# Kernel optimization log

Hardware: AMD Instinct MI355X
Metric: run time of the kernel (lower is better)

The kernel has to match this reference:

```python
import jax, jax.numpy as jnp
import numpy as np

HEADS = 8
DIM_HEAD = 40
SCALE = DIM_HEAD ** -0.5


def setup_inputs() -> dict:
    key = jax.random.key(0)
    ks = jax.random.split(key, 6)
    B, S, D = 2, 4096, 320  # batch, seq (64x64 latent), query_dim
    inner = HEADS * DIM_HEAD  # 320
    s = 0.02
    return {
        "x": jax.random.normal(ks[0], (B, S, D), jnp.float32),
        "Wq": jax.random.normal(ks[1], (inner, D), jnp.float32) * s,
        "Wk": jax.random.normal(ks[2], (inner, D), jnp.float32) * s,
        "Wv": jax.random.normal(ks[3], (inner, D), jnp.float32) * s,
        "Wout": jax.random.normal(ks[4], (D, inner), jnp.float32) * s,
        "bout": jnp.zeros((D,), jnp.float32),
    }


def _split_heads(t):
    # [B, S, h*d] -> [B, h, S, d]
    B, S, _ = t.shape
    return t.reshape(B, S, HEADS, DIM_HEAD).transpose(0, 2, 1, 3)


def reference(x, Wq, Wk, Wv, Wout, bout):
    # self-attention path (context=None): k/v come from x
    q = _split_heads(x @ Wq.T)  # [B,h,S,d]
    k = _split_heads(x @ Wk.T)
    v = _split_heads(x @ Wv.T)
    # scores: materialized O(S^2) attention as in the torch einsum
    attn = jax.nn.softmax(jnp.einsum('bhid,bhjd->bhij', q, k) * SCALE, axis=-1)
    out = jnp.einsum('bhij,bhjd->bhid', attn, v)  # [B,h,S,d]
    B, _, S, _ = out.shape
    out = out.transpose(0, 2, 1, 3).reshape(B, S, HEADS * DIM_HEAD)
    return out @ Wout.T + bout  # to_out (dropout=0 -> identity)
```

## Files before the change

kernel.cpp:

```cpp
#include <hip/hip_runtime.h>

#define HEADS 8
#define DHEAD 40
#define SEQ   4096
#define BATCH 2
#define INNER 320
#define NBH   16
#define QSCALE ((float)(0.15811388300841897 * 1.4426950408889634))

typedef _Float16 f16;
typedef __attribute__((ext_vector_type(2)))  __fp16   fp16x2;
typedef __attribute__((ext_vector_type(4)))  _Float16 half4;
typedef __attribute__((ext_vector_type(8)))  _Float16 half8;
typedef __attribute__((ext_vector_type(16))) float    f32x16;

#if __has_builtin(__builtin_amdgcn_exp2f)
#define EXP2F(x) __builtin_amdgcn_exp2f(x)
#else
#define EXP2F(x) exp2f(x)
#endif

#define MFMA16(a, b, c) __builtin_amdgcn_mfma_f32_32x32x16_f16(a, b, c, 0, 0, 0)

union H8 { half8 h8; fp16x2 p2[4]; uint4 u4; };

#define WQKV4 (3 * INNER * INNER / 4)
#define WOUT4 (INNER * INNER / 4)
#define WTOT4 (WQKV4 + WOUT4)

__global__ __launch_bounds__(256)
void convert_kernel(const float* __restrict__ Wq,
                    const float* __restrict__ Wk,
                    const float* __restrict__ Wv,
                    const float* __restrict__ Wout,
                    f16* __restrict__ wh, f16* __restrict__ wouth)
{
    int i = blockIdx.x * 256 + threadIdx.x;
    if (i >= WTOT4) return;
    float4 v;
    f16* dst;
    float sc = 1.0f;
    if (i < WQKV4) {
        if (i < 25600)      { v = ((const float4*)Wq)[i]; sc = QSCALE; }
        else if (i < 51200) { v = ((const float4*)Wk)[i - 25600]; }
        else                { v = ((const float4*)Wv)[i - 51200]; }
        dst = wh + 4 * (size_t)i;
    } else {
        int j = i - WQKV4;
        v = ((const float4*)Wout)[j];
        dst = wouth + 4 * (size_t)j;
    }
    H8 u;
    u.p2[0] = __builtin_amdgcn_cvt_pkrtz(v.x * sc, v.y * sc);
    u.p2[1] = __builtin_amdgcn_cvt_pkrtz(v.z * sc, v.w * sc);
    *(uint2*)dst = make_uint2(u.u4.x, u.u4.y);
}

#define QSTR 72

__global__ __launch_bounds__(256)
void qkv_gemm_kernel(const float* __restrict__ x, const f16* __restrict__ wh,
                     f16* __restrict__ q, f16* __restrict__ k,
                     f16* __restrict__ vt)
{
    __shared__ f16 lds[(64 + 192) * QSTR];
    f16* As = lds;
    f16* Bs = lds + 64 * QSTR;

    const int tid = threadIdx.x;
    const int nb0 = blockIdx.x * 64;
    const int m0  = blockIdx.y * 64;
    const int wave = tid >> 6, lane = tid & 63, m = lane & 31, half = lane >> 5;
    const int mw = wave >> 1, nw = wave & 1;

    f32x16 acc[3];
    #pragma unroll
    for (int i = 0; i < 16; i++) { acc[0][i] = 0.f; acc[1][i] = 0.f; acc[2][i] = 0.f; }

    for (int k0 = 0; k0 < 320; k0 += 64) {
        __syncthreads();
        #pragma unroll
        for (int u = 0; u < 2; u++) {
            int idx = tid + 256 * u;
            int r = idx >> 3, c8 = idx & 7;
            const float* xr = &x[(size_t)(m0 + r) * 320 + k0 + c8 * 8];
            float4 v0 = *(const float4*)xr;
            float4 v1 = *(const float4*)(xr + 4);
            H8 hh;
            hh.p2[0] = __builtin_amdgcn_cvt_pkrtz(v0.x, v0.y);
            hh.p2[1] = __builtin_amdgcn_cvt_pkrtz(v0.z, v0.w);
            hh.p2[2] = __builtin_amdgcn_cvt_pkrtz(v1.x, v1.y);
            hh.p2[3] = __builtin_amdgcn_cvt_pkrtz(v1.z, v1.w);
            *(uint4*)&As[r * QSTR + c8 * 8] = hh.u4;
        }
        #pragma unroll
        for (int u = 0; u < 6; u++) {
            int idx = tid + 256 * u;
            int r = idx >> 3, c8 = idx & 7;
            int wr = (r >> 6) * 320 + nb0 + (r & 63);
            *(uint4*)&Bs[r * QSTR + c8 * 8] =
                *(const uint4*)&wh[(size_t)wr * 320 + k0 + c8 * 8];
        }
        __syncthreads();
        #pragma unroll
        for (int c = 0; c < 4; c++) {
            half8 a = *(const half8*)&As[(mw * 32 + m) * QSTR + c * 16 + half * 8];
            #pragma unroll
            for (int t = 0; t < 3; t++) {
                half8 bf = *(const half8*)&Bs[(nw * 96 + t * 32 + m) * QSTR + c * 16 + half * 8];
                acc[t] = MFMA16(a, bf, acc[t]);
            }
        }
    }

    const int b = m0 >> 12, s0 = m0 & 4095;

    #pragma unroll
    for (int t = 0; t < 3; t++) {
        int st = nw * 3 + t;
        if (st < 4) {
            f16* dst = (st < 2) ? q : k;
            int col = nb0 + (st & 1) * 32 + m;
            int h  = (col * 205) >> 13;
            int dd = col - h * 40;
            #pragma unroll
            for (int reg = 0; reg < 16; reg++) {
                int crow = 4 * half + (reg & 3) + 8 * (reg >> 2);
                int mg = m0 + mw * 32 + crow;
                int bb = mg >> 12, s = mg & 4095;
                dst[((size_t)(bb * 8 + h) * SEQ + s) * DHEAD + dd] = (f16)acc[t][reg];
            }
        }
    }

    __syncthreads();
    f16* Ct = lds;
    if (nw == 1) {
        #pragma unroll
        for (int t = 1; t < 3; t++) {
            int vr0 = (t - 1) * 32 + m;
            #pragma unroll
            for (int g = 0; g < 4; g++) {
                half4 hh;
                hh.x = (f16)acc[t][4 * g + 0]; hh.y = (f16)acc[t][4 * g + 1];
                hh.z = (f16)acc[t][4 * g + 2]; hh.w = (f16)acc[t][4 * g + 3];
                *(half4*)&Ct[vr0 * QSTR + mw * 32 + 8 * g + 4 * half] = hh;
            }
        }
    }
    __syncthreads();
    #pragma unroll
    for (int u = 0; u < 4; u++) {
        int idx = tid + 256 * u;
        int rl = idx >> 4, c4 = idx & 15;
        int col = nb0 + rl;
        int h  = (col * 205) >> 13;
        int dd = col - h * 40;
        int w4 = c4 & 3;
        int c4p = (c4 & ~3) | ((w4 == 1) ? 2 : (w4 == 2) ? 1 : w4);
        *(uint2*)&vt[((size_t)(b * 8 + h) * DHEAD + dd) * SEQ + s0 + c4p * 4] =
            *(const uint2*)&Ct[rl * QSTR + c4 * 4];
    }
}

__global__ __launch_bounds__(512, 4)
void attn_kernel(const f16* __restrict__ q, const f16* __restrict__ k,
                 const f16* __restrict__ vt, f16* __restrict__ y)
{
    __shared__ __align__(16) unsigned char ldsbuf[33792];
    f16*   ldsh = (f16*)ldsbuf;
    float* ldsf = (float*)ldsbuf;

    const int tid = threadIdx.x;
    const int blk = blockIdx.x;
    const int xcd = blk & 7, slot = blk >> 3;
    const int bh = xcd * 2 + (slot >> 5), qt = slot & 31;
    const int b = bh >> 3, h = bh & 7;
    const int q0 = qt * 128;
    const int wave = tid >> 6, lane = tid & 63, m = lane & 31, half = lane >> 5;
    const int qp = wave >> 1, kh = wave & 1;
    const int x7 = m & 7;

    if (tid < 128) {
        int bsel = tid >> 6, r = tid & 63;
        *(uint4*)&ldsh[bsel * 8192 + r * 64 + 8 * (5 ^ (r & 7))] = make_uint4(0, 0, 0, 0);
    } else {
        int idx = tid - 128;
        int bsel = (idx >= 192) ? 1 : 0;
        int j = idx - bsel * 192;
        int r = 40 + (j >> 3), c = j & 7;
        uint4 val = (r == 40) ? make_uint4(0x3C003C00u, 0x3C003C00u, 0x3C003C00u, 0x3C003C00u)
                              : make_uint4(0, 0, 0, 0);
        *(uint4*)&ldsh[bsel * 8192 + 4096 + r * 64 + 8 * (c ^ (r & 7))] = val;
    }

    half8 zero8;
    #pragma unroll
    for (int j = 0; j < 8; j++) zero8[j] = (f16)0.0f;

    half8 qa[3];
    {
        const f16* qb = q + ((size_t)bh * SEQ + q0 + qp * 32 + m) * DHEAD;
        qa[0] = *(const half8*)&qb[half * 8];
        qa[1] = *(const half8*)&qb[16 + half * 8];
        qa[2] = (half == 1) ? zero8 : *(const half8*)&qb[32];
    }

    f32x16 O0, O1;
    #pragma unroll
    for (int i = 0; i < 16; i++) { O0[i] = 0.f; O1[i] = 0.f; }

    const f16* kb = k  + (size_t)bh * SEQ * DHEAD;
    const f16* vb = vt + (size_t)bh * DHEAD * SEQ;

    const bool aIsK = (tid < 320);
    int adst, astep;
    const f16* aptr;
    if (aIsK) {
        int r = (tid * 205) >> 10, c = tid - r * 5;
        adst = r * 64 + 8 * (c ^ (r & 7));
        aptr = kb + (size_t)r * DHEAD + c * 8;
        astep = 64 * DHEAD;
    } else {
        int t = tid - 320;
        int r = t >> 3, c = t & 7;
        adst = 4096 + r * 64 + 8 * (c ^ (r & 7));
        aptr = vb + (size_t)r * SEQ + c * 8;
        astep = 64;
    }
    const bool hasB = (tid < 128);
    int bdst = 0;
    const f16* bptr = vb;
    if (hasB) {
        int t = 192 + tid;
        int r = t >> 3, c = t & 7;
        bdst = 4096 + r * 64 + 8 * (c ^ (r & 7));
        bptr = vb + (size_t)r * SEQ + c * 8;
    }

    uint4 sA = *(const uint4*)aptr;
    uint4 sB = make_uint4(0, 0, 0, 0);
    if (hasB) sB = *(const uint4*)bptr;

    for (int j0 = 0; j0 < SEQ; j0 += 64) {
        const int stg = ((j0 >> 6) & 1) * 8192;
        *(uint4*)&ldsh[stg + adst] = sA;
        if (hasB) *(uint4*)&ldsh[stg + bdst] = sB;
        __syncthreads();

        if (j0 + 64 < SEQ) {
            aptr += astep;
            sA = *(const uint4*)aptr;
            if (hasB) { bptr += 64; sB = *(const uint4*)bptr; }
        }

        const f16* Kb = &ldsh[stg];
        const f16* Vb = &ldsh[stg + 4096];

        half8 kf[3];
        #pragma unroll
        for (int c = 0; c < 3; c++)
            kf[c] = *(const half8*)&Kb[(kh * 32 + m) * 64 + 8 * ((2 * c + half) ^ x7)];

        f32x16 S;
        #pragma unroll
        for (int i = 0; i < 16; i++) S[i] = 0.f;
        __builtin_amdgcn_s_setprio(1);
        S = MFMA16(kf[0], qa[0], S);
        S = MFMA16(kf[1], qa[1], S);
        S = MFMA16(kf[2], qa[2], S);
        __builtin_amdgcn_s_setprio(0);

        half8 vf[2][2];
        #pragma unroll
        for (int c = 0; c < 2; c++) {
            vf[c][0] = *(const half8*)&Vb[m * 64        + 8 * ((4 * kh + 2 * c + half) ^ x7)];
            vf[c][1] = *(const half8*)&Vb[(32 + m) * 64 + 8 * ((4 * kh + 2 * c + half) ^ x7)];
        }

        H8 p0, p1;
        #pragma unroll
        for (int g = 0; g < 4; g++) {
            p0.p2[g] = __builtin_amdgcn_cvt_pkrtz(EXP2F(S[2 * g]),     EXP2F(S[2 * g + 1]));
            p1.p2[g] = __builtin_amdgcn_cvt_pkrtz(EXP2F(S[8 + 2 * g]), EXP2F(S[9 + 2 * g]));
        }

        __builtin_amdgcn_s_setprio(1);
        O0 = MFMA16(p0.h8, vf[0][0], O0);
        O1 = MFMA16(p0.h8, vf[0][1], O1);
        O0 = MFMA16(p1.h8, vf[1][0], O0);
        O1 = MFMA16(p1.h8, vf[1][1], O1);
        __builtin_amdgcn_s_setprio(0);
    }

    __syncthreads();
    if (kh == 1) {
        #pragma unroll
        for (int reg = 0; reg < 16; reg++) {
            int row = 4 * half + (reg & 3) + 8 * (reg >> 2);
            ldsf[(qp * 32 + row) * 66 + m]      = O0[reg];
            ldsf[(qp * 32 + row) * 66 + 32 + m] = O1[reg];
        }
    }
    __syncthreads();
    if (kh == 0) {
        #pragma unroll
        for (int reg = 0; reg < 16; reg++) {
            int row = 4 * half + (reg & 3) + 8 * (reg >> 2);
            O0[reg] += ldsf[(qp * 32 + row) * 66 + m];
            O1[reg] += ldsf[(qp * 32 + row) * 66 + 32 + m];
        }
        #pragma unroll
        for (int reg = 0; reg < 16; reg++) {
            float l = __shfl(O1[reg], 8 + 32 * half, 64);
            float rinv = 1.0f / l;
            int row = 4 * half + (reg & 3) + 8 * (reg >> 2);
            f16* yr = y + ((size_t)b * SEQ + q0 + qp * 32 + row) * INNER + h * DHEAD;
            yr[m] = (f16)(O0[reg] * rinv);
            if (m < 8) yr[32 + m] = (f16)(O1[reg] * rinv);
        }
    }
}

#define ASTR 72

__global__ __launch_bounds__(256)
void out_proj_kernel(const f16* __restrict__ y, const f16* __restrict__ wouth,
                     const float* __restrict__ bout, float* __restrict__ out)
{
    __shared__ f16 lds[(128 + 64) * ASTR];
    f16* As = lds;
    f16* Bs = lds + 128 * ASTR;

    const int tid = threadIdx.x;
    const int m0 = blockIdx.y * 128;
    const int n0 = blockIdx.x * 64;
    const int wave = tid >> 6, lane = tid & 63, m = lane & 31, half = lane >> 5;

    f32x16 acc[2];
    #pragma unroll
    for (int i = 0; i < 16; i++) { acc[0][i] = 0.f; acc[1][i] = 0.f; }

    for (int k0 = 0; k0 < 320; k0 += 64) {
        __syncthreads();
        #pragma unroll
        for (int u = 0; u < 4; u++) {
            int idx = tid + 256 * u;
            int r = idx >> 3, c8 = idx & 7;
            *(uint4*)&As[r * ASTR + c8 * 8] =
                *(const uint4*)&y[(size_t)(m0 + r) * 320 + k0 + c8 * 8];
        }
        #pragma unroll
        for (int u = 0; u < 2; u++) {
            int idx = tid + 256 * u;
            int r = idx >> 3, c8 = idx & 7;
            *(uint4*)&Bs[r * ASTR + c8 * 8] =
                *(const uint4*)&wouth[(size_t)(n0 + r) * 320 + k0 + c8 * 8];
        }
        __syncthreads();
        #pragma unroll
        for (int c = 0; c < 4; c++) {
            half8 a  = *(const half8*)&As[(wave * 32 + m) * ASTR + c * 16 + half * 8];
            half8 b0 = *(const half8*)&Bs[m * ASTR + c * 16 + half * 8];
            half8 b1 = *(const half8*)&Bs[(32 + m) * ASTR + c * 16 + half * 8];
            acc[0] = MFMA16(a, b0, acc[0]);
            acc[1] = MFMA16(a, b1, acc[1]);
        }
    }

    #pragma unroll
    for (int nt = 0; nt < 2; nt++) {
        int n = n0 + nt * 32 + m;
        float bias = bout[n];
        #pragma unroll
        for (int reg = 0; reg < 16; reg++) {
            int crow = 4 * half + (reg & 3) + 8 * (reg >> 2);
            out[(size_t)(m0 + wave * 32 + crow) * 320 + n] = acc[nt][reg] + bias;
        }
    }
}

extern "C" void kernel_launch(void* const* d_in, const int* in_sizes, int n_in,
                              void* d_out, int out_size, void* d_ws, size_t ws_size,
                              hipStream_t stream)
{
    const float* x    = (const float*)d_in[0];
    const float* Wq   = (const float*)d_in[1];
    const float* Wk   = (const float*)d_in[2];
    const float* Wv   = (const float*)d_in[3];
    const float* Wout = (const float*)d_in[4];
    const float* bout = (const float*)d_in[5];
    float* out = (float*)d_out;

    unsigned char* ws = (unsigned char*)d_ws;
    f16* wh    = (f16*)(ws);
    f16* wouth = (f16*)(ws +   614400);
    f16* qd    = (f16*)(ws +   819200);
    f16* kd    = (f16*)(ws +  6062080);
    f16* vtd   = (f16*)(ws + 11304960);
    f16* yd    = (f16*)(ws + 16547840);

    convert_kernel <<<400,          256, 0, stream>>>(Wq, Wk, Wv, Wout, wh, wouth);
    qkv_gemm_kernel<<<dim3(5, 128), 256, 0, stream>>>(x, wh, qd, kd, vtd);
    attn_kernel    <<<512,          512, 0, stream>>>(qd, kd, vtd, yd);
    out_proj_kernel<<<dim3(5, 64),  256, 0, stream>>>(yd, wouth, bout, out);
}
```

Before: 159.5 us.

## Double KV tile to 128 keys per iteration in attention loop

Each attention-loop iteration now stages 128 keys instead of 64, so each wave computes two 32-key score blocks and runs eight PV MFMAs per barrier. The aim is to halve the number of __syncthreads and loop iterations and give more independent MFMA work to overlap with exp. In exchange, LDS grows from 33 KB to 64 KB per block and register pressure rises, which may cut occupancy below the declared 4 blocks per CU.

```diff
diff --git a/kernel.cpp b/kernel.cpp
--- a/kernel.cpp
+++ b/kernel.cpp
@@ -167,7 +167,7 @@
 void attn_kernel(const f16* __restrict__ q, const f16* __restrict__ k,
                  const f16* __restrict__ vt, f16* __restrict__ y)
 {
-    __shared__ __align__(16) unsigned char ldsbuf[33792];
+    __shared__ __align__(16) unsigned char ldsbuf[65536];
     f16*   ldsh = (f16*)ldsbuf;
     float* ldsf = (float*)ldsbuf;
 
@@ -181,17 +181,25 @@
     const int qp = wave >> 1, kh = wave & 1;
     const int x7 = m & 7;
 
-    if (tid < 128) {
-        int bsel = tid >> 6, r = tid & 63;
-        *(uint4*)&ldsh[bsel * 8192 + r * 64 + 8 * (5 ^ (r & 7))] = make_uint4(0, 0, 0, 0);
-    } else {
-        int idx = tid - 128;
-        int bsel = (idx >= 192) ? 1 : 0;
-        int j = idx - bsel * 192;
-        int r = 40 + (j >> 3), c = j & 7;
-        uint4 val = (r == 40) ? make_uint4(0x3C003C00u, 0x3C003C00u, 0x3C003C00u, 0x3C003C00u)
-                              : make_uint4(0, 0, 0, 0);
-        *(uint4*)&ldsh[bsel * 8192 + 4096 + r * 64 + 8 * (c ^ (r & 7))] = val;
+    if (tid < 256) {
+        int bsel = tid >> 7, r = tid & 127;
+        *(uint4*)&ldsh[bsel * 16384 + r * 64 + 8 * (5 ^ (r & 7))] = make_uint4(0, 0, 0, 0);
+    }
+    {
+        int idx = tid;
+        #pragma unroll
+        for (int pass = 0; pass < 2; pass++) {
+            if (pass == 0 || tid < 256) {
+                int bsel = (idx >= 384) ? 1 : 0;
+                int j = idx - 384 * bsel;
+                int r = 40 + (j >> 4), c = j & 15;
+                uint4 val = (r == 40) ? make_uint4(0x3C003C00u, 0x3C003C00u, 0x3C003C00u, 0x3C003C00u)
+                                      : make_uint4(0, 0, 0, 0);
+                *(uint4*)&ldsh[bsel * 16384 + 8192 + r * 128
+                               + 8 * ((c & 8) | ((c & 7) ^ (r & 7)))] = val;
+            }
+            idx = 512 + tid;
+        }
     }
 
     half8 zero8;
@@ -213,83 +221,100 @@
     const f16* kb = k  + (size_t)bh * SEQ * DHEAD;
     const f16* vb = vt + (size_t)bh * DHEAD * SEQ;
 
-    const bool aIsK = (tid < 320);
-    int adst, astep;
-    const f16* aptr;
-    if (aIsK) {
-        int r = (tid * 205) >> 10, c = tid - r * 5;
-        adst = r * 64 + 8 * (c ^ (r & 7));
-        aptr = kb + (size_t)r * DHEAD + c * 8;
-        astep = 64 * DHEAD;
+    int r0s = (tid * 205) >> 10, c0s = tid - r0s * 5;
+    const int d0 = r0s * 64 + 8 * (c0s ^ (r0s & 7));
+    const f16* p0 = kb + (size_t)r0s * DHEAD + c0s * 8;
+
+    int d1; const f16* p1; int st1;
+    if (tid < 128) {
+        int s = 512 + tid;
+        int r = (s * 205) >> 10, c = s - r * 5;
+        d1 = r * 64 + 8 * (c ^ (r & 7));
+        p1 = kb + (size_t)r * DHEAD + c * 8;
+        st1 = 128 * DHEAD;
     } else {
-        int t = tid - 320;
-        int r = t >> 3, c = t & 7;
-        adst = 4096 + r * 64 + 8 * (c ^ (r & 7));
-        aptr = vb + (size_t)r * SEQ + c * 8;
-        astep = 64;
-    }
-    const bool hasB = (tid < 128);
-    int bdst = 0;
-    const f16* bptr = vb;
-    if (hasB) {
-        int t = 192 + tid;
-        int r = t >> 3, c = t & 7;
-        bdst = 4096 + r * 64 + 8 * (c ^ (r & 7));
-        bptr = vb + (size_t)r * SEQ + c * 8;
-    }
-
-    uint4 sA = *(const uint4*)aptr;
-    uint4 sB = make_uint4(0, 0, 0, 0);
-    if (hasB) sB = *(const uint4*)bptr;
-
-    for (int j0 = 0; j0 < SEQ; j0 += 64) {
-        const int stg = ((j0 >> 6) & 1) * 8192;
-        *(uint4*)&ldsh[stg + adst] = sA;
-        if (hasB) *(uint4*)&ldsh[stg + bdst] = sB;
+        int t = tid - 128;
+        int r = t >> 4, c = t & 15;
+        d1 = 8192 + r * 128 + 8 * ((c & 8) | ((c & 7) ^ (r & 7)));
+        p1 = vb + (size_t)r * SEQ + c * 8;
+        st1 = 128;
+    }
+    const bool has2 = (tid < 256);
+    int d2 = 0; const f16* p2 = vb;
+    if (has2) {
+        int t = 384 + tid;
+        int r = t >> 4, c = t & 15;
+        d2 = 8192 + r * 128 + 8 * ((c & 8) | ((c & 7) ^ (r & 7)));
+        p2 = vb + (size_t)r * SEQ + c * 8;
+    }
+
+    uint4 s0v = *(const uint4*)p0;
+    uint4 s1v = *(const uint4*)p1;
+    uint4 s2v = make_uint4(0, 0, 0, 0);
+    if (has2) s2v = *(const uint4*)p2;
+
+    for (int j0 = 0; j0 < SEQ; j0 += 128) {
+        const int stg = ((j0 >> 7) & 1) * 16384;
+        *(uint4*)&ldsh[stg + d0] = s0v;
+        *(uint4*)&ldsh[stg + d1] = s1v;
+        if (has2) *(uint4*)&ldsh[stg + d2] = s2v;
         __syncthreads();
 
-        if (j0 + 64 < SEQ) {
-            aptr += astep;
-            sA = *(const uint4*)aptr;
-            if (hasB) { bptr += 64; sB = *(const uint4*)bptr; }
+        if (j0 + 128 < SEQ) {
+            p0 += 128 * DHEAD; s0v = *(const uint4*)p0;
+            p1 += st1;         s1v = *(const uint4*)p1;
+            if (has2) { p2 += 128; s2v = *(const uint4*)p2; }
         }
 
         const f16* Kb = &ldsh[stg];
-        const f16* Vb = &ldsh[stg + 4096];
-
-        half8 kf[3];
-        #pragma unroll
-        for (int c = 0; c < 3; c++)
-            kf[c] = *(const half8*)&Kb[(kh * 32 + m) * 64 + 8 * ((2 * c + half) ^ x7)];
-
-        f32x16 S;
-        #pragma unroll
-        for (int i = 0; i < 16; i++) S[i] = 0.f;
+        const f16* Vb = &ldsh[stg + 8192];
+
+        half8 kfA[3], kfB[3];
+        #pragma unroll
+        for (int c = 0; c < 3; c++) {
+            kfA[c] = *(const half8*)&Kb[(kh * 64 + m) * 64      + 8 * ((2 * c + half) ^ x7)];
+            kfB[c] = *(const half8*)&Kb[(kh * 64 + 32 + m) * 64 + 8 * ((2 * c + half) ^ x7)];
+        }
+
+        f32x16 SA, SB;
+        #pragma unroll
+        for (int i = 0; i < 16; i++) { SA[i] = 0.f; SB[i] = 0.f; }
         __builtin_amdgcn_s_setprio(1);
-        S = MFMA16(kf[0], qa[0], S);
-        S = MFMA16(kf[1], qa[1], S);
-        S = MFMA16(kf[2], qa[2], S);
+        SA = MFMA16(kfA[0], qa[0], SA);  SB = MFMA16(kfB[0], qa[0], SB);
+        SA = MFMA16(kfA[1], qa[1], SA);  SB = MFMA16(kfB[1], qa[1], SB);
+        SA = MFMA16(kfA[2], qa[2], SA);  SB = MFMA16(kfB[2], qa[2], SB);
         __builtin_amdgcn_s_setprio(0);
 
-        half8 vf[2][2];
+        half8 vfA[2][2], vfB[2][2];
         #pragma unroll
         for (int c = 0; c < 2; c++) {
-            vf[c][0] = *(const half8*)&Vb[m * 64        + 8 * ((4 * kh + 2 * c + half) ^ x7)];
-            vf[c][1] = *(const half8*)&Vb[(32 + m) * 64 + 8 * ((4 * kh + 2 * c + half) ^ x7)];
-        }
-
-        H8 p0, p1;
+            int chA = kh * 8 + 2 * c + half;
+            int chB = chA + 4;
+            int sA = (chA & 8) | ((chA & 7) ^ x7);
+            int sB = (chB & 8) | ((chB & 7) ^ x7);
+            vfA[c][0] = *(const half8*)&Vb[m * 128        + 8 * sA];
+            vfA[c][1] = *(const half8*)&Vb[(32 + m) * 128 + 8 * sA];
+            vfB[c][0] = *(const half8*)&Vb[m * 128        + 8 * sB];
+            vfB[c][1] = *(const half8*)&Vb[(32 + m) * 128 + 8 * sB];
+        }
+
+        H8 pA0, pA1, pB0, pB1;
         #pragma unroll
         for (int g = 0; g < 4; g++) {
-            p0.p2[g] = __builtin_amdgcn_cvt_pkrtz(EXP2F(S[2 * g]),     EXP2F(S[2 * g + 1]));
-            p1.p2[g] = __builtin_amdgcn_cvt_pkrtz(EXP2F(S[8 + 2 * g]), EXP2F(S[9 + 2 * g]));
+            pA0.p2[g] = __builtin_amdgcn_cvt_pkrtz(EXP2F(SA[2 * g]),     EXP2F(SA[2 * g + 1]));
+            pA1.p2[g] = __builtin_amdgcn_cvt_pkrtz(EXP2F(SA[8 + 2 * g]), EXP2F(SA[9 + 2 * g]));
+        }
+        #pragma unroll
+        for (int g = 0; g < 4; g++) {
+            pB0.p2[g] = __builtin_amdgcn_cvt_pkrtz(EXP2F(SB[2 * g]),     EXP2F(SB[2 * g + 1]));
+            pB1.p2[g] = __builtin_amdgcn_cvt_pkrtz(EXP2F(SB[8 + 2 * g]), EXP2F(SB[9 + 2 * g]));
         }
 
         __builtin_amdgcn_s_setprio(1);
-        O0 = MFMA16(p0.h8, vf[0][0], O0);
-        O1 = MFMA16(p0.h8, vf[0][1], O1);
-        O0 = MFMA16(p1.h8, vf[1][0], O0);
-        O1 = MFMA16(p1.h8, vf[1][1], O1);
+        O0 = MFMA16(pA0.h8, vfA[0][0], O0);  O1 = MFMA16(pA0.h8, vfA[0][1], O1);
+        O0 = MFMA16(pA1.h8, vfA[1][0], O0);  O1 = MFMA16(pA1.h8, vfA[1][1], O1);
+        O0 = MFMA16(pB0.h8, vfB[0][0], O0);  O1 = MFMA16(pB0.h8, vfB[0][1], O1);
+        O0 = MFMA16(pB1.h8, vfB[1][0], O0);  O1 = MFMA16(pB1.h8, vfB[1][1], O1);
         __builtin_amdgcn_s_setprio(0);
     }
 
```

After: 194.9 us. +22.2%, slower.

## Software-pipeline attention loop: overlap PV MFMA of previous tile with QK of current

Applied to the files above, without the earlier changes.

Restructures the attention main loop so that the exp/pack of probabilities for tile j overlaps with the QK^T MFMAs of tile j+1, and the PV MFMAs consume the previous tile's P. This needs a triple-buffered LDS stage (48 KB instead of ~33 KB) so the V tile stays live one extra iteration, plus a peeled prologue and epilogue. The aim is to hide exp latency behind matrix ops. The cost is more LDS per block, which may reduce occupancy below the launch-bounds target of 4 blocks per CU.

```diff
diff --git a/kernel.cpp b/kernel.cpp
--- a/kernel.cpp
+++ b/kernel.cpp
@@ -167,7 +167,7 @@
 void attn_kernel(const f16* __restrict__ q, const f16* __restrict__ k,
                  const f16* __restrict__ vt, f16* __restrict__ y)
 {
-    __shared__ __align__(16) unsigned char ldsbuf[33792];
+    __shared__ __align__(16) unsigned char ldsbuf[49152];
     f16*   ldsh = (f16*)ldsbuf;
     float* ldsf = (float*)ldsbuf;
 
@@ -181,17 +181,24 @@
     const int qp = wave >> 1, kh = wave & 1;
     const int x7 = m & 7;
 
-    if (tid < 128) {
+    if (tid < 192) {
         int bsel = tid >> 6, r = tid & 63;
         *(uint4*)&ldsh[bsel * 8192 + r * 64 + 8 * (5 ^ (r & 7))] = make_uint4(0, 0, 0, 0);
-    } else {
-        int idx = tid - 128;
-        int bsel = (idx >= 192) ? 1 : 0;
-        int j = idx - bsel * 192;
-        int r = 40 + (j >> 3), c = j & 7;
-        uint4 val = (r == 40) ? make_uint4(0x3C003C00u, 0x3C003C00u, 0x3C003C00u, 0x3C003C00u)
-                              : make_uint4(0, 0, 0, 0);
-        *(uint4*)&ldsh[bsel * 8192 + 4096 + r * 64 + 8 * (c ^ (r & 7))] = val;
+    }
+    {
+        int idx = tid;
+        #pragma unroll
+        for (int pass = 0; pass < 2; pass++) {
+            if (pass == 0 || tid < 64) {
+                int bsel = idx / 192;
+                int j = idx - bsel * 192;
+                int r = 40 + (j >> 3), c = j & 7;
+                uint4 val = (r == 40) ? make_uint4(0x3C003C00u, 0x3C003C00u, 0x3C003C00u, 0x3C003C00u)
+                                      : make_uint4(0, 0, 0, 0);
+                *(uint4*)&ldsh[bsel * 8192 + 4096 + r * 64 + 8 * (c ^ (r & 7))] = val;
+            }
+            idx = 512 + tid;
+        }
     }
 
     half8 zero8;
@@ -242,26 +249,21 @@
     uint4 sB = make_uint4(0, 0, 0, 0);
     if (hasB) sB = *(const uint4*)bptr;
 
-    for (int j0 = 0; j0 < SEQ; j0 += 64) {
-        const int stg = ((j0 >> 6) & 1) * 8192;
+    H8 p0, p1;
+    int stg  = 0;
+    int stgv = 0;
+
+    {
         *(uint4*)&ldsh[stg + adst] = sA;
         if (hasB) *(uint4*)&ldsh[stg + bdst] = sB;
         __syncthreads();
-
-        if (j0 + 64 < SEQ) {
-            aptr += astep;
-            sA = *(const uint4*)aptr;
-            if (hasB) { bptr += 64; sB = *(const uint4*)bptr; }
-        }
-
-        const f16* Kb = &ldsh[stg];
-        const f16* Vb = &ldsh[stg + 4096];
+        aptr += astep; sA = *(const uint4*)aptr;
+        if (hasB) { bptr += 64; sB = *(const uint4*)bptr; }
 
         half8 kf[3];
         #pragma unroll
         for (int c = 0; c < 3; c++)
-            kf[c] = *(const half8*)&Kb[(kh * 32 + m) * 64 + 8 * ((2 * c + half) ^ x7)];
-
+            kf[c] = *(const half8*)&ldsh[stg + (kh * 32 + m) * 64 + 8 * ((2 * c + half) ^ x7)];
         f32x16 S;
         #pragma unroll
         for (int i = 0; i < 16; i++) S[i] = 0.f;
@@ -270,27 +272,75 @@
         S = MFMA16(kf[1], qa[1], S);
         S = MFMA16(kf[2], qa[2], S);
         __builtin_amdgcn_s_setprio(0);
-
+        #pragma unroll
+        for (int g = 0; g < 4; g++) {
+            p0.p2[g] = __builtin_amdgcn_cvt_pkrtz(EXP2F(S[2 * g]),     EXP2F(S[2 * g + 1]));
+            p1.p2[g] = __builtin_amdgcn_cvt_pkrtz(EXP2F(S[8 + 2 * g]), EXP2F(S[9 + 2 * g]));
+        }
+        stg = 8192;
+    }
+
+    for (int j = 1; j < 64; ++j) {
+        *(uint4*)&ldsh[stg + adst] = sA;
+        if (hasB) *(uint4*)&ldsh[stg + bdst] = sB;
+        __syncthreads();
+
+        if (j < 63) {
+            aptr += astep; sA = *(const uint4*)aptr;
+            if (hasB) { bptr += 64; sB = *(const uint4*)bptr; }
+        }
+
+        half8 kf[3];
+        #pragma unroll
+        for (int c = 0; c < 3; c++)
+            kf[c] = *(const half8*)&ldsh[stg + (kh * 32 + m) * 64 + 8 * ((2 * c + half) ^ x7)];
+        f32x16 S;
+        #pragma unroll
+        for (int i = 0; i < 16; i++) S[i] = 0.f;
+        __builtin_amdgcn_s_setprio(1);
+        S = MFMA16(kf[0], qa[0], S);
+        S = MFMA16(kf[1], qa[1], S);
+        S = MFMA16(kf[2], qa[2], S);
+        __builtin_amdgcn_s_setprio(0);
+
+        {
+            const f16* Vb = &ldsh[stgv + 4096];
+            half8 vf[2][2];
+            #pragma unroll
+            for (int c = 0; c < 2; c++) {
+                vf[c][0] = *(const half8*)&Vb[m * 64        + 8 * ((4 * kh + 2 * c + half) ^ x7)];
+                vf[c][1] = *(const half8*)&Vb[(32 + m) * 64 + 8 * ((4 * kh + 2 * c + half) ^ x7)];
+            }
+            __builtin_amdgcn_s_setprio(1);
+            O0 = MFMA16(p0.h8, vf[0][0], O0);
+            O1 = MFMA16(p0.h8, vf[0][1], O1);
+            O0 = MFMA16(p1.h8, vf[1][0], O0);
+            O1 = MFMA16(p1.h8, vf[1][1], O1);
+            __builtin_amdgcn_s_setprio(0);
+        }
+
+        #pragma unroll
+        for (int g = 0; g < 4; g++) {
+            p0.p2[g] = __builtin_amdgcn_cvt_pkrtz(EXP2F(S[2 * g]),     EXP2F(S[2 * g + 1]));
+            p1.p2[g] = __builtin_amdgcn_cvt_pkrtz(EXP2F(S[8 + 2 * g]), EXP2F(S[9 + 2 * g]));
+        }
+
+        stgv = stg;
+        stg = (stg == 16384) ? 0 : stg + 8192;
+    }
+
+    {
+        const f16* Vb = &ldsh[stgv + 4096];
         half8 vf[2][2];
         #pragma unroll
         for (int c = 0; c < 2; c++) {
             vf[c][0] = *(const half8*)&Vb[m * 64        + 8 * ((4 * kh + 2 * c + half) ^ x7)];
             vf[c][1] = *(const half8*)&Vb[(32 + m) * 64 + 8 * ((4 * kh + 2 * c + half) ^ x7)];
         }
-
-        H8 p0, p1;
-        #pragma unroll
-        for (int g = 0; g < 4; g++) {
-            p0.p2[g] = __builtin_amdgcn_cvt_pkrtz(EXP2F(S[2 * g]),     EXP2F(S[2 * g + 1]));
-            p1.p2[g] = __builtin_amdgcn_cvt_pkrtz(EXP2F(S[8 + 2 * g]), EXP2F(S[9 + 2 * g]));
-        }
-
-        __builtin_amdgcn_s_setprio(1);
         O0 = MFMA16(p0.h8, vf[0][0], O0);
         O1 = MFMA16(p0.h8, vf[0][1], O1);
         O0 = MFMA16(p1.h8, vf[1][0], O0);
         O1 = MFMA16(p1.h8, vf[1][1], O1);
-        __builtin_amdgcn_s_setprio(0);
     }
 
     __syncthreads();
```

New measurement: 156.4 us (median of 3 runs). About the same (-1.9%).

## Software-pipeline attention loop: overlap QK^T of next tile with exp and PV

Applied to the files above, without the earlier changes.

Restructures the attention main loop into a two-deep software pipeline: the S=QK^T MFMAs for tile j+1 are issued before the exp and PV MFMAs of tile j, alternating between two S accumulators. LDS staging grows from 2 to 4 buffers (64 KB) so tiles still being read by PV are not overwritten, and the constant-padding init is extended to all four buffers. The aim is to hide exp/convert latency behind matrix-core work. In exchange, LDS use and register pressure rise, which may reduce occupancy (launch bounds request 4 blocks of 512 threads).

```diff
diff --git a/kernel.cpp b/kernel.cpp
--- a/kernel.cpp
+++ b/kernel.cpp
@@ -167,7 +167,7 @@
 void attn_kernel(const f16* __restrict__ q, const f16* __restrict__ k,
                  const f16* __restrict__ vt, f16* __restrict__ y)
 {
-    __shared__ __align__(16) unsigned char ldsbuf[33792];
+    __shared__ __align__(16) unsigned char ldsbuf[65536];
     f16*   ldsh = (f16*)ldsbuf;
     float* ldsf = (float*)ldsbuf;
 
@@ -181,17 +181,24 @@
     const int qp = wave >> 1, kh = wave & 1;
     const int x7 = m & 7;
 
-    if (tid < 128) {
+    if (tid < 256) {
         int bsel = tid >> 6, r = tid & 63;
         *(uint4*)&ldsh[bsel * 8192 + r * 64 + 8 * (5 ^ (r & 7))] = make_uint4(0, 0, 0, 0);
-    } else {
-        int idx = tid - 128;
-        int bsel = (idx >= 192) ? 1 : 0;
-        int j = idx - bsel * 192;
-        int r = 40 + (j >> 3), c = j & 7;
-        uint4 val = (r == 40) ? make_uint4(0x3C003C00u, 0x3C003C00u, 0x3C003C00u, 0x3C003C00u)
-                              : make_uint4(0, 0, 0, 0);
-        *(uint4*)&ldsh[bsel * 8192 + 4096 + r * 64 + 8 * (c ^ (r & 7))] = val;
+    }
+    {
+        int idx = tid;
+        #pragma unroll
+        for (int pass = 0; pass < 2; pass++) {
+            if (pass == 0 || tid < 256) {
+                int bsel = idx / 192;
+                int j = idx - bsel * 192;
+                int r = 40 + (j >> 3), c = j & 7;
+                uint4 val = (r == 40) ? make_uint4(0x3C003C00u, 0x3C003C00u, 0x3C003C00u, 0x3C003C00u)
+                                      : make_uint4(0, 0, 0, 0);
+                *(uint4*)&ldsh[bsel * 8192 + 4096 + r * 64 + 8 * (c ^ (r & 7))] = val;
+            }
+            idx = 512 + tid;
+        }
     }
 
     half8 zero8;
@@ -242,56 +249,72 @@
     uint4 sB = make_uint4(0, 0, 0, 0);
     if (hasB) sB = *(const uint4*)bptr;
 
-    for (int j0 = 0; j0 < SEQ; j0 += 64) {
-        const int stg = ((j0 >> 6) & 1) * 8192;
-        *(uint4*)&ldsh[stg + adst] = sA;
-        if (hasB) *(uint4*)&ldsh[stg + bdst] = sB;
-        __syncthreads();
-
-        if (j0 + 64 < SEQ) {
-            aptr += astep;
-            sA = *(const uint4*)aptr;
-            if (hasB) { bptr += 64; sB = *(const uint4*)bptr; }
-        }
-
-        const f16* Kb = &ldsh[stg];
-        const f16* Vb = &ldsh[stg + 4096];
-
-        half8 kf[3];
-        #pragma unroll
-        for (int c = 0; c < 3; c++)
-            kf[c] = *(const half8*)&Kb[(kh * 32 + m) * 64 + 8 * ((2 * c + half) ^ x7)];
-
-        f32x16 S;
-        #pragma unroll
-        for (int i = 0; i < 16; i++) S[i] = 0.f;
-        __builtin_amdgcn_s_setprio(1);
-        S = MFMA16(kf[0], qa[0], S);
-        S = MFMA16(kf[1], qa[1], S);
-        S = MFMA16(kf[2], qa[2], S);
-        __builtin_amdgcn_s_setprio(0);
-
-        half8 vf[2][2];
-        #pragma unroll
-        for (int c = 0; c < 2; c++) {
-            vf[c][0] = *(const half8*)&Vb[m * 64        + 8 * ((4 * kh + 2 * c + half) ^ x7)];
-            vf[c][1] = *(const half8*)&Vb[(32 + m) * 64 + 8 * ((4 * kh + 2 * c + half) ^ x7)];
-        }
-
-        H8 p0, p1;
-        #pragma unroll
-        for (int g = 0; g < 4; g++) {
-            p0.p2[g] = __builtin_amdgcn_cvt_pkrtz(EXP2F(S[2 * g]),     EXP2F(S[2 * g + 1]));
-            p1.p2[g] = __builtin_amdgcn_cvt_pkrtz(EXP2F(S[8 + 2 * g]), EXP2F(S[9 + 2 * g]));
-        }
-
-        __builtin_amdgcn_s_setprio(1);
-        O0 = MFMA16(p0.h8, vf[0][0], O0);
-        O1 = MFMA16(p0.h8, vf[0][1], O1);
-        O0 = MFMA16(p1.h8, vf[1][0], O0);
-        O1 = MFMA16(p1.h8, vf[1][1], O1);
-        __builtin_amdgcn_s_setprio(0);
-    }
+    H8 p0, p1;
+    f32x16 Sa, Sb;
+
+#define STAGE_S(jj, SC) do {                                                  \
+    const int stg_ = ((jj) & 3) * 8192;                                       \
+    *(uint4*)&ldsh[stg_ + adst] = sA;                                         \
+    if (hasB) *(uint4*)&ldsh[stg_ + bdst] = sB;                               \
+    __syncthreads();                                                          \
+    if ((jj) + 1 < 64) {                                                      \
+        aptr += astep; sA = *(const uint4*)aptr;                              \
+        if (hasB) { bptr += 64; sB = *(const uint4*)bptr; }                   \
+    }                                                                         \
+    half8 kf0_ = *(const half8*)&ldsh[stg_ + (kh * 32 + m) * 64 + 8 * ((0 + half) ^ x7)]; \
+    half8 kf1_ = *(const half8*)&ldsh[stg_ + (kh * 32 + m) * 64 + 8 * ((2 + half) ^ x7)]; \
+    half8 kf2_ = *(const half8*)&ldsh[stg_ + (kh * 32 + m) * 64 + 8 * ((4 + half) ^ x7)]; \
+    _Pragma("unroll")                                                         \
+    for (int i_ = 0; i_ < 16; i_++) SC[i_] = 0.f;                             \
+    __builtin_amdgcn_s_setprio(1);                                            \
+    SC = MFMA16(kf0_, qa[0], SC);                                             \
+    SC = MFMA16(kf1_, qa[1], SC);                                             \
+    SC = MFMA16(kf2_, qa[2], SC);                                             \
+    __builtin_amdgcn_s_setprio(0);                                            \
+} while (0)
+
+#define PVSTEP(jv) do {                                                       \
+    const f16* Vb_ = &ldsh[(((jv) & 3) * 8192) + 4096];                       \
+    half8 v00_ = *(const half8*)&Vb_[m * 64        + 8 * ((4 * kh + 0 + half) ^ x7)]; \
+    half8 v01_ = *(const half8*)&Vb_[(32 + m) * 64 + 8 * ((4 * kh + 0 + half) ^ x7)]; \
+    half8 v10_ = *(const half8*)&Vb_[m * 64        + 8 * ((4 * kh + 2 + half) ^ x7)]; \
+    half8 v11_ = *(const half8*)&Vb_[(32 + m) * 64 + 8 * ((4 * kh + 2 + half) ^ x7)]; \
+    __builtin_amdgcn_s_setprio(1);                                            \
+    O0 = MFMA16(p0.h8, v00_, O0);                                             \
+    O1 = MFMA16(p0.h8, v01_, O1);                                             \
+    O0 = MFMA16(p1.h8, v10_, O0);                                             \
+    O1 = MFMA16(p1.h8, v11_, O1);                                             \
+    __builtin_amdgcn_s_setprio(0);                                            \
+} while (0)
+
+#define EXPSTEP(SE) do {                                                      \
+    _Pragma("unroll")                                                         \
+    for (int g_ = 0; g_ < 4; g_++) {                                          \
+        p0.p2[g_] = __builtin_amdgcn_cvt_pkrtz(EXP2F(SE[2 * g_]),     EXP2F(SE[2 * g_ + 1])); \
+        p1.p2[g_] = __builtin_amdgcn_cvt_pkrtz(EXP2F(SE[8 + 2 * g_]), EXP2F(SE[9 + 2 * g_])); \
+    }                                                                         \
+} while (0)
+
+    STAGE_S(0, Sa);
+    STAGE_S(1, Sb);
+    EXPSTEP(Sa);
+
+    for (int j = 2; j < 64; j += 2) {
+        STAGE_S(j, Sa);
+        PVSTEP(j - 2);
+        EXPSTEP(Sb);
+        STAGE_S(j + 1, Sb);
+        PVSTEP(j - 1);
+        EXPSTEP(Sa);
+    }
+
+    PVSTEP(62);
+    EXPSTEP(Sb);
+    PVSTEP(63);
+
+#undef STAGE_S
+#undef PVSTEP
+#undef EXPSTEP
 
     __syncthreads();
     if (kh == 1) {
```

New measurement: 170.6 us. 7.0% more time.
